# Kernel optimization log

Hardware: AMD Instinct MI355X
Metric: run time of the kernel (lower is better)

The kernel has to match this reference:

```python
import jax, jax.numpy as jnp
import numpy as np

D_MODEL = 768
NUM_HEADS = 12
DEPTH = D_MODEL // NUM_HEADS
HIDDEN = int(D_MODEL * 4.0)
LN_EPS = 1e-5


def layer_norm(x, g, b):
    mu = jnp.mean(x, axis=-1, keepdims=True)
    var = jnp.mean(jnp.square(x - mu), axis=-1, keepdims=True)
    return (x - mu) * jax.lax.rsqrt(var + LN_EPS) * g + b


def setup_inputs() -> dict:
    key = jax.random.key(0)
    ks = jax.random.split(key, 8)
    s = 0.02
    return {
        "x": jax.random.normal(ks[0], (2, 2048, D_MODEL), dtype=jnp.float32),
        "ln1_g": jnp.ones((D_MODEL,), jnp.float32),
        "ln1_b": jnp.zeros((D_MODEL,), jnp.float32),
        "w_qkv": jax.random.normal(ks[1], (D_MODEL, 3 * D_MODEL), jnp.float32) * s,
        "b_qkv": jnp.zeros((3 * D_MODEL,), jnp.float32),
        "w_proj": jax.random.normal(ks[2], (D_MODEL, D_MODEL), jnp.float32) * s,
        "b_proj": jnp.zeros((D_MODEL,), jnp.float32),
        "ln2_g": jnp.ones((D_MODEL,), jnp.float32),
        "ln2_b": jnp.zeros((D_MODEL,), jnp.float32),
        "w1": jax.random.normal(ks[3], (D_MODEL, HIDDEN), jnp.float32) * s,
        "b1": jnp.zeros((HIDDEN,), jnp.float32),
        "w2": jax.random.normal(ks[4], (HIDDEN, D_MODEL), jnp.float32) * s,
        "b2": jnp.zeros((D_MODEL,), jnp.float32),
    }


def reference(x, ln1_g, ln1_b, w_qkv, b_qkv, w_proj, b_proj, ln2_g, ln2_b, w1, b1, w2, b2):
    B, N, C = x.shape
    # --- MHA branch (pre-norm) ---
    h = layer_norm(x, ln1_g, ln1_b)
    qkv = h @ w_qkv + b_qkv                             # [B,N,3C]
    qkv = qkv.reshape(B, N, NUM_HEADS, DEPTH, 3)
    qkv = jnp.transpose(qkv, (4, 0, 2, 1, 3))           # [3,B,H,N,D]
    q, k, v = qkv[0], qkv[1], qkv[2]
    scale = 1.0 / jnp.sqrt(jnp.asarray(DEPTH, x.dtype))
    attn = jnp.einsum('bhnd,bhmd->bhnm', q, k) * scale  # [B,H,N,N]
    attn = jax.nn.softmax(attn, axis=-1)
    o = jnp.einsum('bhnm,bhmd->bhnd', attn, v)          # [B,H,N,D]
    o = jnp.transpose(o, (0, 2, 1, 3)).reshape(B, N, C)
    o = o @ w_proj + b_proj
    x = x + o
    # --- MLP branch (pre-norm) ---
    h = layer_norm(x, ln2_g, ln2_b)
    h = jax.nn.gelu(h @ w1 + b1, approximate=False)
    h = h @ w2 + b2
    return x + h
```

## Files before the change

### kernel.cpp

```cpp
#include <hip/hip_runtime.h>

typedef unsigned short u16;
typedef __attribute__((ext_vector_type(8))) short short8;
typedef __attribute__((ext_vector_type(4))) float float4v;

#define TOK 4096
#define CDIM 768
#define NHEAD 12
#define DHEAD 64
#define HID 3072
#define SEQ 2048
#define BHTOT 24

#define QSCALE 0.18033688011112042f

__device__ __forceinline__ u16 f2bf(float f) {
  unsigned int u = __builtin_bit_cast(unsigned int, f);
  u = (u + 0x7fffu + ((u >> 16) & 1u)) >> 16;
  return (u16)u;
}

#define GLD16(gaddr, laddr)                                                    \
  __builtin_amdgcn_global_load_lds(                                            \
      (const __attribute__((address_space(1))) unsigned int*)(gaddr),          \
      (__attribute__((address_space(3))) unsigned int*)(laddr), 16, 0, 0)

template <int NCHUNK>
__device__ __forceinline__ void stage_swz(const u16* __restrict__ gbase,
                                          int grs, u16* lds, int tid) {
#pragma unroll
  for (int c = 0; c < NCHUNK; ++c) {
    int off = c * 4096 + tid * 16;
    int row = off >> 7;
    int colb = (off & 127) ^ ((row & 7) << 4);
    GLD16(gbase + (size_t)row * grs + (colb >> 1), (char*)lds + off);
  }
}

__device__ __forceinline__ short8 lds_frag(const u16* lds, int row, int cb) {
  return *(const short8*)((const char*)lds +
                          ((row << 7) | (cb ^ ((row & 7) << 4))));
}

__global__ __launch_bounds__(256) void transpose_cast(
    const float* __restrict__ in, u16* __restrict__ out, int K, int Nw) {
  __shared__ float tile[32][33];
  int n0 = blockIdx.x * 32, k0 = blockIdx.y * 32;
  int tx = threadIdx.x, ty = threadIdx.y;
#pragma unroll
  for (int i = 0; i < 4; ++i)
    tile[ty + i * 8][tx] = in[(size_t)(k0 + ty + i * 8) * Nw + n0 + tx];
  __syncthreads();
#pragma unroll
  for (int i = 0; i < 4; ++i)
    out[(size_t)(n0 + ty + i * 8) * K + k0 + tx] = f2bf(tile[tx][ty + i * 8]);
}

__global__ __launch_bounds__(256) void ln_kernel(
    const float* __restrict__ x, const float* __restrict__ gam,
    const float* __restrict__ bet, u16* __restrict__ out) {
  int row = blockIdx.x;
  int t = threadIdx.x;
  const float* xr = x + (size_t)row * CDIM;
  float v0 = xr[t], v1 = xr[t + 256], v2 = xr[t + 512];
  float s = v0 + v1 + v2;
  __shared__ float red[16];
  int lane = t & 63, wid = t >> 6;
#pragma unroll
  for (int off = 32; off; off >>= 1) s += __shfl_down(s, off);
  if (lane == 0) red[wid] = s;
  __syncthreads();
  if (t == 0) red[8] = (red[0] + red[1] + red[2] + red[3]) * (1.f / CDIM);
  __syncthreads();
  float mu = red[8];
  float d0 = v0 - mu, d1 = v1 - mu, d2 = v2 - mu;
  float q = d0 * d0 + d1 * d1 + d2 * d2;
#pragma unroll
  for (int off = 32; off; off >>= 1) q += __shfl_down(q, off);
  if (lane == 0) red[4 + wid] = q;
  __syncthreads();
  if (t == 0) {
    float var = (red[4] + red[5] + red[6] + red[7]) * (1.f / CDIM);
    red[9] = rsqrtf(var + 1e-5f);
  }
  __syncthreads();
  float rstd = red[9];
  u16* orow = out + (size_t)row * CDIM;
  orow[t] = f2bf(d0 * rstd * gam[t] + bet[t]);
  orow[t + 256] = f2bf(d1 * rstd * gam[t + 256] + bet[t + 256]);
  orow[t + 512] = f2bf(d2 * rstd * gam[t + 512] + bet[t + 512]);
}

template <int EPI, int BM, int BN, int DB>
__global__ __launch_bounds__(256) void gemm_bt(
    const u16* __restrict__ A, const u16* __restrict__ BT,
    const float* __restrict__ bias, const float* __restrict__ res,
    float* __restrict__ outf, u16* __restrict__ ob0, u16* __restrict__ ob1,
    u16* __restrict__ ob2, int K) {
  constexpr int MR = BM / 32, NR = BN / 32;
  constexpr int NBUF = DB ? 2 : 1;
  __shared__ u16 As[NBUF][BM * 64];
  __shared__ u16 Bs[NBUF][BN * 64];
  int tid = threadIdx.x;
  int gx = gridDim.x;
  int nwg = gx * (int)gridDim.y;
  int flat = blockIdx.y * gx + blockIdx.x;
  int qq = nwg >> 3, rr = nwg & 7;
  int xcd = flat & 7, rest = flat >> 3;
  int swz = (xcd < rr ? xcd * (qq + 1) : rr * (qq + 1) + (xcd - rr) * qq) + rest;
  int row0 = (swz / gx) * BM, col0 = (swz % gx) * BN;
  int wid = tid >> 6, lane = tid & 63;
  int wm = wid >> 1, wn = wid & 1;
  int rbase = wm * (BM / 2), cbase = wn * (BN / 2);
  int r = lane & 15, g = lane >> 4;
  float4v zero = {0.f, 0.f, 0.f, 0.f};
  float4v acc[MR][NR];
#pragma unroll
  for (int m = 0; m < MR; ++m)
#pragma unroll
    for (int n = 0; n < NR; ++n) acc[m][n] = zero;
  const int nk = K >> 6;
  if (DB) {
    stage_swz<BM / 32>(A + (size_t)row0 * K, K, As[0], tid);
    stage_swz<BN / 32>(BT + (size_t)col0 * K, K, Bs[0], tid);
  }
  for (int k = 0; k < nk; ++k) {
    const u16* Ac;
    const u16* Bc;
    if (DB) {
      Ac = As[k & 1];
      Bc = Bs[k & 1];
      if (k + 1 < nk) {
        stage_swz<BM / 32>(A + (size_t)row0 * K + (k + 1) * 64, K,
                           As[(k + 1) & 1], tid);
        stage_swz<BN / 32>(BT + (size_t)col0 * K + (k + 1) * 64, K,
                           Bs[(k + 1) & 1], tid);
        asm volatile("s_waitcnt vmcnt(4)" ::: "memory");
      } else {
        asm volatile("s_waitcnt vmcnt(0)" ::: "memory");
      }
      __builtin_amdgcn_s_barrier();
    } else {
      Ac = As[0];
      Bc = Bs[0];
      stage_swz<BM / 32>(A + (size_t)row0 * K + k * 64, K, As[0], tid);
      stage_swz<BN / 32>(BT + (size_t)col0 * K + k * 64, K, Bs[0], tid);
      __syncthreads();
    }
#pragma unroll
    for (int kk = 0; kk < 2; ++kk) {
      short8 av[MR], bv[NR];
#pragma unroll
      for (int m = 0; m < MR; ++m)
        av[m] = lds_frag(Ac, rbase + m * 16 + r, kk * 64 + g * 16);
#pragma unroll
      for (int n = 0; n < NR; ++n)
        bv[n] = lds_frag(Bc, cbase + n * 16 + r, kk * 64 + g * 16);
#pragma unroll
      for (int m = 0; m < MR; ++m)
#pragma unroll
        for (int n = 0; n < NR; ++n)
          acc[m][n] = __builtin_amdgcn_mfma_f32_16x16x32_bf16(av[m], bv[n],
                                                              acc[m][n], 0, 0, 0);
    }
    if (DB)
      __builtin_amdgcn_s_barrier();
    else
      __syncthreads();
  }
#pragma unroll
  for (int m = 0; m < MR; ++m) {
#pragma unroll
    for (int n = 0; n < NR; ++n) {
#pragma unroll
      for (int j = 0; j < 4; ++j) {
        int row = row0 + rbase + m * 16 + g * 4 + j;
        int col = col0 + cbase + n * 16 + r;
        float v = acc[m][n][j] + bias[col];
        if (EPI == 0) {
          int sdx = col % 3;
          int hd = col / 3;
          int h = hd >> 6, d = hd & 63;
          int b = row >> 11, nn = row & 2047;
          if (sdx == 0)
            ob0[(((size_t)(b * NHEAD + h) * SEQ + nn) << 6) + d] =
                f2bf(v * QSCALE);
          else if (sdx == 1)
            ob1[(((size_t)(b * NHEAD + h) * SEQ + nn) << 6) + d] = f2bf(v);
          else
            ob2[(((size_t)(b * NHEAD + h) * DHEAD + d) << 11) + nn] = f2bf(v);
        } else if (EPI == 1 || EPI == 3) {
          outf[(size_t)row * CDIM + col] = res[(size_t)row * CDIM + col] + v;
        } else if (EPI == 2) {
          float ge = 0.5f * v * (1.f + erff(v * 0.70710678118f));
          ob0[(size_t)row * HID + col] = f2bf(ge);
        }
      }
    }
  }
}

__global__ __launch_bounds__(256) void attn_kernel(
    const u16* __restrict__ Qb, const u16* __restrict__ Kb,
    const u16* __restrict__ Vt, float* __restrict__ Op,
    float* __restrict__ ml) {
  __shared__ u16 Ks[2][64 * 64];
  __shared__ u16 Vs[2][64 * 64];
  __shared__ u16 Ps[4][32 * 64];
  int tid = threadIdx.x, wid = tid >> 6, lane = tid & 63;
  int r = lane & 15, g = lane >> 4;
  int bh = blockIdx.y;
  int half = blockIdx.x >> 4, qblk = blockIdx.x & 15;
  const u16* Qh = Qb + (size_t)bh * SEQ * DHEAD;
  const u16* Kh = Kb + (size_t)bh * SEQ * DHEAD + (size_t)half * 1024 * DHEAD;
  const u16* Vh = Vt + (size_t)bh * DHEAD * SEQ + half * 1024;
  int qr0 = qblk * 128 + wid * 32;
  short8 qa[2][2];
#pragma unroll
  for (int qg = 0; qg < 2; ++qg) {
    qa[qg][0] =
        *(const short8*)(&Qh[(size_t)(qr0 + qg * 16 + r) * DHEAD + g * 8]);
    qa[qg][1] =
        *(const short8*)(&Qh[(size_t)(qr0 + qg * 16 + r) * DHEAD + 32 + g * 8]);
  }
  short8 vones;
#pragma unroll
  for (int i = 0; i < 8; ++i) vones[i] = (short)0x3F80;
  float4v zero = {0.f, 0.f, 0.f, 0.f};
  float4v oacc[2][4];
  float4v accsum[2];
#pragma unroll
  for (int qg = 0; qg < 2; ++qg) {
    accsum[qg] = zero;
#pragma unroll
    for (int nd = 0; nd < 4; ++nd) oacc[qg][nd] = zero;
  }
  u16* Pw = &Ps[wid][0];
  stage_swz<2>(Kh, DHEAD, Ks[0], tid);
  stage_swz<2>(Vh, SEQ, Vs[0], tid);
  __syncthreads();
  for (int t0 = 0; t0 < 1024; t0 += 64) {
    int cur = (t0 >> 6) & 1;
    const u16* Kc = Ks[cur];
    const u16* Vc = Vs[cur];
    if (t0 + 64 < 1024) {
      stage_swz<2>(Kh + (size_t)(t0 + 64) * DHEAD, DHEAD, Ks[cur ^ 1], tid);
      stage_swz<2>(Vh + (t0 + 64), SEQ, Vs[cur ^ 1], tid);
    }
    float4v s[2][4];
#pragma unroll
    for (int qg = 0; qg < 2; ++qg)
#pragma unroll
      for (int n = 0; n < 4; ++n) s[qg][n] = zero;
#pragma unroll
    for (int kk = 0; kk < 2; ++kk) {
      short8 av[4];
#pragma unroll
      for (int n = 0; n < 4; ++n)
        av[n] = lds_frag(Kc, n * 16 + r, kk * 64 + g * 16);
      __builtin_amdgcn_s_setprio(1);
#pragma unroll
      for (int qg = 0; qg < 2; ++qg)
#pragma unroll
        for (int n = 0; n < 4; ++n)
          s[qg][n] = __builtin_amdgcn_mfma_f32_16x16x32_bf16(
              av[n], qa[qg][kk], s[qg][n], 0, 0, 0);
      __builtin_amdgcn_s_setprio(0);
    }
#pragma unroll
    for (int qg = 0; qg < 2; ++qg) {
#pragma unroll
      for (int n = 0; n < 4; ++n) {
        float p[4];
#pragma unroll
        for (int j = 0; j < 4; ++j) {
          float e = s[qg][n][j];
          asm("v_exp_f32 %0, %1" : "=v"(p[j]) : "v"(e));
        }
        unsigned int wlo, whi;
        asm("v_cvt_pk_bf16_f32 %0, %1, %2" : "=v"(wlo) : "v"(p[0]), "v"(p[1]));
        asm("v_cvt_pk_bf16_f32 %0, %1, %2" : "=v"(whi) : "v"(p[2]), "v"(p[3]));
        uint2 w2;
        w2.x = wlo;
        w2.y = whi;
        *(uint2*)((char*)Pw + qg * 2048 +
                  ((r << 7) | ((n * 32 + g * 8) ^ ((r & 7) << 4)))) = w2;
      }
    }
#pragma unroll
    for (int kk = 0; kk < 2; ++kk) {
      short8 bv[4];
#pragma unroll
      for (int nd = 0; nd < 4; ++nd)
        bv[nd] = lds_frag(Vc, nd * 16 + r, kk * 64 + g * 16);
      short8 pa[2];
#pragma unroll
      for (int qg = 0; qg < 2; ++qg)
        pa[qg] = lds_frag(Pw + qg * 1024, r, kk * 64 + g * 16);
      __builtin_amdgcn_s_setprio(1);
#pragma unroll
      for (int qg = 0; qg < 2; ++qg) {
#pragma unroll
        for (int nd = 0; nd < 4; ++nd)
          oacc[qg][nd] = __builtin_amdgcn_mfma_f32_16x16x32_bf16(
              pa[qg], bv[nd], oacc[qg][nd], 0, 0, 0);
        accsum[qg] = __builtin_amdgcn_mfma_f32_16x16x32_bf16(
            pa[qg], vones, accsum[qg], 0, 0, 0);
      }
      __builtin_amdgcn_s_setprio(0);
    }
    __syncthreads();
  }
  size_t obase = ((size_t)(half * BHTOT + bh) * SEQ);
#pragma unroll
  for (int qg = 0; qg < 2; ++qg) {
#pragma unroll
    for (int nd = 0; nd < 4; ++nd)
#pragma unroll
      for (int j = 0; j < 4; ++j) {
        int rowq = qr0 + qg * 16 + g * 4 + j;
        Op[(obase + rowq) * DHEAD + nd * 16 + r] = oacc[qg][nd][j];
      }
    if (r == 0) {
#pragma unroll
      for (int j = 0; j < 4; ++j) {
        int rowq = qr0 + qg * 16 + g * 4 + j;
        ml[obase + rowq] = accsum[qg][j];
      }
    }
  }
}

__global__ __launch_bounds__(256) void attn_combine(
    const float* __restrict__ Op, const float* __restrict__ ml,
    u16* __restrict__ aO) {
  int t = threadIdx.x;
  int idx = blockIdx.x * 4 + (t >> 6);
  int d = t & 63;
  int bh = idx >> 11, row = idx & 2047;
  int b = bh / NHEAD, h = bh - b * NHEAD;
  float l0 = ml[idx];
  float l1 = ml[(size_t)BHTOT * SEQ + idx];
  float o0 = Op[(size_t)idx * DHEAD + d];
  float o1 = Op[((size_t)BHTOT * SEQ + idx) * DHEAD + d];
  float val = (o0 + o1) / (l0 + l1);
  aO[(size_t)(b * SEQ + row) * CDIM + h * DHEAD + d] = f2bf(val);
}

extern "C" void kernel_launch(void* const* d_in, const int* in_sizes, int n_in,
                              void* d_out, int out_size, void* d_ws,
                              size_t ws_size, hipStream_t stream) {
  const float* x = (const float*)d_in[0];
  const float* ln1g = (const float*)d_in[1];
  const float* ln1b = (const float*)d_in[2];
  const float* wqkv = (const float*)d_in[3];
  const float* bqkv = (const float*)d_in[4];
  const float* wproj = (const float*)d_in[5];
  const float* bproj = (const float*)d_in[6];
  const float* ln2g = (const float*)d_in[7];
  const float* ln2b = (const float*)d_in[8];
  const float* w1 = (const float*)d_in[9];
  const float* b1 = (const float*)d_in[10];
  const float* w2 = (const float*)d_in[11];
  const float* b2 = (const float*)d_in[12];
  float* out = (float*)d_out;

  char* ws = (char*)d_ws;
  size_t o = 0;
  auto nxt = [&](size_t bytes) -> void* {
    void* p = ws + o;
    o += (bytes + 255) & ~(size_t)255;
    return p;
  };
  u16* wqkvT = (u16*)nxt((size_t)2304 * 768 * 2);
  u16* wprojT = (u16*)nxt((size_t)768 * 768 * 2);
  u16* w1T = (u16*)nxt((size_t)3072 * 768 * 2);
  u16* w2T = (u16*)nxt((size_t)768 * 3072 * 2);
  u16* h1 = (u16*)nxt((size_t)TOK * CDIM * 2);
  u16* Qb = (u16*)nxt((size_t)TOK * CDIM * 2);
  u16* Kb = (u16*)nxt((size_t)TOK * CDIM * 2);
  u16* Vt = (u16*)nxt((size_t)TOK * CDIM * 2);
  u16* aO = (u16*)nxt((size_t)TOK * CDIM * 2);
  float* y1 = (float*)nxt((size_t)TOK * CDIM * 4);
  u16* h2 = (u16*)nxt((size_t)TOK * CDIM * 2);
  u16* mh = (u16*)nxt((size_t)TOK * HID * 2);
  float* ml = (float*)nxt((size_t)2 * BHTOT * SEQ * 4);
  float* Op = (float*)mh;

  dim3 tb(32, 8);
  transpose_cast<<<dim3(2304 / 32, 768 / 32), tb, 0, stream>>>(wqkv, wqkvT, 768, 2304);
  transpose_cast<<<dim3(768 / 32, 768 / 32), tb, 0, stream>>>(wproj, wprojT, 768, 768);
  transpose_cast<<<dim3(3072 / 32, 768 / 32), tb, 0, stream>>>(w1, w1T, 768, 3072);
  transpose_cast<<<dim3(768 / 32, 3072 / 32), tb, 0, stream>>>(w2, w2T, 3072, 768);

  ln_kernel<<<TOK, 256, 0, stream>>>(x, ln1g, ln1b, h1);

  gemm_bt<0, 128, 96, 0><<<dim3(2304 / 96, TOK / 128), 256, 0, stream>>>(
      h1, wqkvT, bqkv, nullptr, nullptr, Qb, Kb, Vt, 768);

  attn_kernel<<<dim3(32, BHTOT), 256, 0, stream>>>(Qb, Kb, Vt, Op, ml);
  attn_combine<<<BHTOT * SEQ / 4, 256, 0, stream>>>(Op, ml, aO);

  gemm_bt<1, 64, 64, 1><<<dim3(768 / 64, TOK / 64), 256, 0, stream>>>(
      aO, wprojT, bproj, x, y1, nullptr, nullptr, nullptr, 768);

  ln_kernel<<<TOK, 256, 0, stream>>>(y1, ln2g, ln2b, h2);

  gemm_bt<2, 128, 128, 0><<<dim3(3072 / 128, TOK / 128), 256, 0, stream>>>(
      h2, w1T, b1, nullptr, nullptr, mh, nullptr, nullptr, 768);

  gemm_bt<3, 64, 64, 1><<<dim3(768 / 64, TOK / 64), 256, 0, stream>>>(
      mh, w2T, b2, y1, out, nullptr, nullptr, nullptr, 3072);
}
```

Measured before the change: 179.3 us.

## Merge weight transposes, store attention partials as bf16, double-buffer MLP1 GEMM

Folds the four weight transpose-cast launches into one kernel that dispatches on block index. Writes the split-K attention partial outputs as bf16 instead of fp32, halving combine-stage traffic at some precision cost. Switches the first MLP GEMM to a 128x64 double-buffered tile, with the vmcnt wait chosen from the per-stage load count.

```diff
diff --git a/kernel.cpp b/kernel.cpp
--- a/kernel.cpp
+++ b/kernel.cpp
@@ -19,6 +19,10 @@
   u = (u + 0x7fffu + ((u >> 16) & 1u)) >> 16;
   return (u16)u;
 }
+__device__ __forceinline__ float bf2f(u16 v) {
+  unsigned int u = ((unsigned int)v) << 16;
+  return __builtin_bit_cast(float, u);
+}
 
 #define GLD16(gaddr, laddr)                                                    \
   __builtin_amdgcn_global_load_lds(                                            \
@@ -42,10 +46,27 @@
                           ((row << 7) | (cb ^ ((row & 7) << 4))));
 }
 
-__global__ __launch_bounds__(256) void transpose_cast(
-    const float* __restrict__ in, u16* __restrict__ out, int K, int Nw) {
+__global__ __launch_bounds__(256) void transpose_cast_all(
+    const float* __restrict__ w0, const float* __restrict__ wp,
+    const float* __restrict__ wm1, const float* __restrict__ wm2,
+    u16* __restrict__ o0, u16* __restrict__ op, u16* __restrict__ om1,
+    u16* __restrict__ om2) {
   __shared__ float tile[32][33];
-  int n0 = blockIdx.x * 32, k0 = blockIdx.y * 32;
+  int t = blockIdx.x;
+  const float* in;
+  u16* out;
+  int K, Nw, ti;
+  if (t < 1728) {
+    in = w0; out = o0; K = 768; Nw = 2304; ti = t;
+  } else if (t < 2304) {
+    in = wp; out = op; K = 768; Nw = 768; ti = t - 1728;
+  } else if (t < 4608) {
+    in = wm1; out = om1; K = 768; Nw = 3072; ti = t - 2304;
+  } else {
+    in = wm2; out = om2; K = 3072; Nw = 768; ti = t - 4608;
+  }
+  int ntx = Nw >> 5;
+  int n0 = (ti % ntx) * 32, k0 = (ti / ntx) * 32;
   int tx = threadIdx.x, ty = threadIdx.y;
 #pragma unroll
   for (int i = 0; i < 4; ++i)
@@ -99,6 +120,7 @@
     u16* __restrict__ ob2, int K) {
   constexpr int MR = BM / 32, NR = BN / 32;
   constexpr int NBUF = DB ? 2 : 1;
+  constexpr int NL = BM / 32 + BN / 32;
   __shared__ u16 As[NBUF][BM * 64];
   __shared__ u16 Bs[NBUF][BN * 64];
   int tid = threadIdx.x;
@@ -135,7 +157,12 @@
                            As[(k + 1) & 1], tid);
         stage_swz<BN / 32>(BT + (size_t)col0 * K + (k + 1) * 64, K,
                            Bs[(k + 1) & 1], tid);
-        asm volatile("s_waitcnt vmcnt(4)" ::: "memory");
+        if constexpr (NL == 4)
+          asm volatile("s_waitcnt vmcnt(4)" ::: "memory");
+        else if constexpr (NL == 6)
+          asm volatile("s_waitcnt vmcnt(6)" ::: "memory");
+        else
+          asm volatile("s_waitcnt vmcnt(0)" ::: "memory");
       } else {
         asm volatile("s_waitcnt vmcnt(0)" ::: "memory");
       }
@@ -202,7 +229,7 @@
 
 __global__ __launch_bounds__(256) void attn_kernel(
     const u16* __restrict__ Qb, const u16* __restrict__ Kb,
-    const u16* __restrict__ Vt, float* __restrict__ Op,
+    const u16* __restrict__ Vt, u16* __restrict__ Op,
     float* __restrict__ ml) {
   __shared__ u16 Ks[2][64 * 64];
   __shared__ u16 Vs[2][64 * 64];
@@ -319,7 +346,7 @@
 #pragma unroll
       for (int j = 0; j < 4; ++j) {
         int rowq = qr0 + qg * 16 + g * 4 + j;
-        Op[(obase + rowq) * DHEAD + nd * 16 + r] = oacc[qg][nd][j];
+        Op[(obase + rowq) * DHEAD + nd * 16 + r] = f2bf(oacc[qg][nd][j]);
       }
     if (r == 0) {
 #pragma unroll
@@ -332,7 +359,7 @@
 }
 
 __global__ __launch_bounds__(256) void attn_combine(
-    const float* __restrict__ Op, const float* __restrict__ ml,
+    const u16* __restrict__ Op, const float* __restrict__ ml,
     u16* __restrict__ aO) {
   int t = threadIdx.x;
   int idx = blockIdx.x * 4 + (t >> 6);
@@ -341,8 +368,8 @@
   int b = bh / NHEAD, h = bh - b * NHEAD;
   float l0 = ml[idx];
   float l1 = ml[(size_t)BHTOT * SEQ + idx];
-  float o0 = Op[(size_t)idx * DHEAD + d];
-  float o1 = Op[((size_t)BHTOT * SEQ + idx) * DHEAD + d];
+  float o0 = bf2f(Op[(size_t)idx * DHEAD + d]);
+  float o1 = bf2f(Op[((size_t)BHTOT * SEQ + idx) * DHEAD + d]);
   float val = (o0 + o1) / (l0 + l1);
   aO[(size_t)(b * SEQ + row) * CDIM + h * DHEAD + d] = f2bf(val);
 }
@@ -385,13 +412,10 @@
   u16* h2 = (u16*)nxt((size_t)TOK * CDIM * 2);
   u16* mh = (u16*)nxt((size_t)TOK * HID * 2);
   float* ml = (float*)nxt((size_t)2 * BHTOT * SEQ * 4);
-  float* Op = (float*)mh;
-
-  dim3 tb(32, 8);
-  transpose_cast<<<dim3(2304 / 32, 768 / 32), tb, 0, stream>>>(wqkv, wqkvT, 768, 2304);
-  transpose_cast<<<dim3(768 / 32, 768 / 32), tb, 0, stream>>>(wproj, wprojT, 768, 768);
-  transpose_cast<<<dim3(3072 / 32, 768 / 32), tb, 0, stream>>>(w1, w1T, 768, 3072);
-  transpose_cast<<<dim3(768 / 32, 3072 / 32), tb, 0, stream>>>(w2, w2T, 3072, 768);
+  u16* Op = (u16*)mh;
+
+  transpose_cast_all<<<6912, dim3(32, 8), 0, stream>>>(
+      wqkv, wproj, w1, w2, wqkvT, wprojT, w1T, w2T);
 
   ln_kernel<<<TOK, 256, 0, stream>>>(x, ln1g, ln1b, h1);
 
@@ -406,7 +430,7 @@
 
   ln_kernel<<<TOK, 256, 0, stream>>>(y1, ln2g, ln2b, h2);
 
-  gemm_bt<2, 128, 128, 0><<<dim3(3072 / 128, TOK / 128), 256, 0, stream>>>(
+  gemm_bt<2, 128, 64, 1><<<dim3(3072 / 64, TOK / 128), 256, 0, stream>>>(
       h2, w1T, b1, nullptr, nullptr, mh, nullptr, nullptr, 768);
 
   gemm_bt<3, 64, 64, 1><<<dim3(768 / 64, TOK / 64), 256, 0, stream>>>(
```

After: 174.3 us. 1.03x faster.
